# Kernel optimization log

Hardware: AMD Instinct MI355X
Metric: run time of the kernel (lower is better)

## Reference

```python
import jax, jax.numpy as jnp
import numpy as np

NEG_INF = -1e30  # stands in for -inf on the H-diagonal (matches softmax zeroing)


def conv1x1(x, W, b):
    # x: [B,C,H,W], W: [O,C], b: [O] -> [B,O,H,W]
    return jnp.einsum('bchw,oc->bohw', x, W) + b[None, :, None, None]


def setup_inputs() -> dict:
    key = jax.random.key(0)
    ks = jax.random.split(key, 8)
    B, C, H, W = 4, 64, 256, 256
    C8 = C // 8
    s = 1.0 / np.sqrt(C)
    return {
        'x': jax.random.normal(ks[0], (B, C, H, W), jnp.float32),
        'Wq': jax.random.normal(ks[1], (C8, C), jnp.float32) * s,
        'bq': jnp.zeros((C8,), jnp.float32),
        'Wk': jax.random.normal(ks[2], (C8, C), jnp.float32) * s,
        'bk': jnp.zeros((C8,), jnp.float32),
        'Wv': jax.random.normal(ks[3], (C, C), jnp.float32) * s,
        'bv': jnp.zeros((C,), jnp.float32),
        'gamma': jnp.zeros((1,), jnp.float32),
    }


def reference(x, Wq, bq, Wk, bk, Wv, bv, gamma):
    B, C, H, W = x.shape
    q = conv1x1(x, Wq, bq)   # [B,C8,H,W]
    k = conv1x1(x, Wk, bk)   # [B,C8,H,W]
    v = conv1x1(x, Wv, bv)   # [B,C,H,W]

    # Row (height-axis) attention energies with -inf on the self (diagonal) entry.
    energy_H = jnp.einsum('bchw,bcjw->bhwj', q, k)               # [B,H,W,H]
    diag = jnp.eye(H, dtype=bool)[:, None, :]                    # [H,1,H]
    energy_H = jnp.where(diag[None], NEG_INF, energy_H)
    # Column (width-axis) attention energies.
    energy_W = jnp.einsum('bchw,bchj->bhwj', q, k)               # [B,H,W,W]

    att = jax.nn.softmax(jnp.concatenate([energy_H, energy_W], axis=3), axis=3)
    att_H, att_W = att[..., :H], att[..., H:]                    # [B,H,W,H], [B,H,W,W]

    out_H = jnp.einsum('bcjw,bhwj->bchw', v, att_H)
    out_W = jnp.einsum('bchj,bhwj->bchw', v, att_W)
    return gamma[0] * (out_H + out_W) + x
```

## Files before the change

kernel.cpp:

```cpp
#include <hip/hip_runtime.h>

#define Bn 4
#define Cn 64
#define Hn 256
#define Wn 256
#define HWn 65536

typedef unsigned int u32;
typedef __attribute__((ext_vector_type(2))) unsigned int u32x2;
typedef __attribute__((ext_vector_type(8))) short bf16x8;
typedef __attribute__((ext_vector_type(4))) float f32x4;
typedef __attribute__((ext_vector_type(16))) float f32x16;

__device__ __forceinline__ unsigned short f2b(float f) {
    union { float f; unsigned u; } v; v.f = f;
    return (unsigned short)(v.u >> 16);
}
__device__ __forceinline__ float b2f(unsigned short s) {
    union { float f; unsigned u; } v; v.u = ((unsigned)s) << 16;
    return v.f;
}
__device__ __forceinline__ u32 cvtpk(float lo, float hi) {
    u32 r;
    asm("v_cvt_pk_bf16_f32 %0, %1, %2" : "=v"(r) : "v"(lo), "v"(hi));
    return r;
}
__device__ __forceinline__ void vswap(u32& a, u32& b) {
    asm volatile("v_permlane32_swap_b32 %0, %1" : "+v"(a), "+v"(b));
}
__device__ __forceinline__ float pair_other(float v, int lane) {
    union { float f; u32 u; } A; A.f = v;
    u32 a = A.u, b = A.u;
    vswap(a, b);
    union { u32 u; float f; } R; R.u = (lane < 32) ? b : a;
    return R.f;
}
__device__ __forceinline__ bf16x8 expPack(const f32x16& e, int base, float& ss) {
    float p0 = __expf(e[base + 0]), p1 = __expf(e[base + 1]);
    u32 A = cvtpk(p0, p1); ss += p0 + p1;
    float p4 = __expf(e[base + 4]), p5 = __expf(e[base + 5]);
    u32 B = cvtpk(p4, p5); ss += p4 + p5;
    vswap(A, B);
    float p2 = __expf(e[base + 2]), p3 = __expf(e[base + 3]);
    u32 C = cvtpk(p2, p3); ss += p2 + p3;
    float p6 = __expf(e[base + 6]), p7 = __expf(e[base + 7]);
    u32 D = cvtpk(p6, p7); ss += p6 + p7;
    vswap(C, D);
    union { u32 w[4]; bf16x8 v; } u;
    u.w[0] = A; u.w[1] = C; u.w[2] = B; u.w[3] = D;
    return u.v;
}

__global__ __launch_bounds__(256) void k_proj(
    const float* __restrict__ x,
    const float* __restrict__ Wq, const float* __restrict__ bq,
    const float* __restrict__ Wk, const float* __restrict__ bk,
    const float* __restrict__ Wv, const float* __restrict__ bv,
    unsigned short* __restrict__ qbr, unsigned short* __restrict__ kbr,
    unsigned short* __restrict__ v_row)
{
    __shared__ __align__(16) char Xl[2][16384];
    int t = threadIdx.x, lane = t & 63, wv = t >> 6;
    int row16 = lane & 15, g = lane >> 4;
    int u0 = blockIdx.x * 4;

    bf16x8 Af[5][2];
    #pragma unroll
    for (int m = 0; m < 5; ++m) {
        const float* wrow;
        if (m == 0) wrow = (row16 < 8) ? (Wq + row16 * 64) : (Wk + (row16 - 8) * 64);
        else        wrow = Wv + (size_t)((m - 1) * 16 + row16) * 64;
        #pragma unroll
        for (int ks = 0; ks < 2; ++ks) {
            int c0 = ks * 32 + g * 8;
            f32x4 w0 = *(const f32x4*)(wrow + c0);
            f32x4 w1 = *(const f32x4*)(wrow + c0 + 4);
            bf16x8 a;
            a[0] = (short)f2b(w0[0]); a[1] = (short)f2b(w0[1]);
            a[2] = (short)f2b(w0[2]); a[3] = (short)f2b(w0[3]);
            a[4] = (short)f2b(w1[0]); a[5] = (short)f2b(w1[1]);
            a[6] = (short)f2b(w1[2]); a[7] = (short)f2b(w1[3]);
            Af[m][ks] = a;
        }
    }

    int px4 = (t & 31) * 4;
    int cbase = (t >> 5) << 2;

    f32x4 st[2][8];
    {
        int u = u0;
        int b = u >> 9, rest = u & 511, h = rest >> 1, half = rest & 1;
        const float* xb2 = x + (size_t)b * Cn * HWn + (size_t)h * Wn + half * 128;
        #pragma unroll
        for (int pass = 0; pass < 2; ++pass) {
            int c0s = cbase + pass * 32;
            #pragma unroll
            for (int j = 0; j < 4; ++j)
                st[0][pass * 4 + j] = *(const f32x4*)(xb2 + (size_t)(c0s + j) * HWn + px4);
        }
    }

    #pragma unroll
    for (int ui = 0; ui < 4; ++ui) {
        int u = u0 + ui;
        int b = u >> 9, rest = u & 511, h = rest >> 1, half = rest & 1;
        int cur = ui & 1;

        #pragma unroll
        for (int pass = 0; pass < 2; ++pass) {
            int c0s = cbase + pass * 32;
            #pragma unroll
            for (int i = 0; i < 4; ++i) {
                int px = px4 + i;
                u32x2 w;
                w[0] = (u32)f2b(st[cur][pass * 4 + 0][i]) | ((u32)f2b(st[cur][pass * 4 + 1][i]) << 16);
                w[1] = (u32)f2b(st[cur][pass * 4 + 2][i]) | ((u32)f2b(st[cur][pass * 4 + 3][i]) << 16);
                unsigned addr = (unsigned)(px * 128)
                              + (((unsigned)(c0s * 2)) ^ ((((unsigned)px >> 3) & 7) << 4));
                *(u32x2*)(Xl[cur] + addr) = w;
            }
        }
        __syncthreads();

        if (ui < 3) {
            int un = u + 1;
            int bn = un >> 9, restn = un & 511, hn = restn >> 1, halfn = restn & 1;
            const float* xb2 = x + (size_t)bn * Cn * HWn + (size_t)hn * Wn + halfn * 128;
            #pragma unroll
            for (int pass = 0; pass < 2; ++pass) {
                int c0s = cbase + pass * 32;
                #pragma unroll
                for (int j = 0; j < 4; ++j)
                    st[cur ^ 1][pass * 4 + j] = *(const f32x4*)(xb2 + (size_t)(c0s + j) * HWn + px4);
            }
        }

        f32x4 acc[5][2];
        #pragma unroll
        for (int m = 0; m < 5; ++m)
            #pragma unroll
            for (int nt = 0; nt < 2; ++nt)
                acc[m][nt] = (f32x4){0.f, 0.f, 0.f, 0.f};

        #pragma unroll
        for (int nt = 0; nt < 2; ++nt) {
            int px = wv * 32 + nt * 16 + row16;
            #pragma unroll
            for (int ks = 0; ks < 2; ++ks) {
                int c0 = ks * 32 + g * 8;
                unsigned addr = (unsigned)(px * 128)
                              + (((unsigned)(c0 * 2)) ^ ((((unsigned)px >> 3) & 7) << 4));
                bf16x8 bf = *(const bf16x8*)(Xl[cur] + addr);
                #pragma unroll
                for (int m = 0; m < 5; ++m)
                    acc[m][nt] = __builtin_amdgcn_mfma_f32_16x16x32_bf16(Af[m][ks], bf, acc[m][nt], 0, 0, 0);
            }
        }

        f32x4 bQK = (g < 2) ? *(const f32x4*)(bq + g * 4)
                            : *(const f32x4*)(bk + (g - 2) * 4);
        #pragma unroll
        for (int nt = 0; nt < 2; ++nt) {
            int p = half * 128 + wv * 32 + nt * 16 + row16;
            f32x4 d = acc[0][nt];
            d[0] += bQK[0]; d[1] += bQK[1]; d[2] += bQK[2]; d[3] += bQK[3];
            u32 w0 = (u32)f2b(d[0]) | ((u32)f2b(d[1]) << 16);
            u32 w1 = (u32)f2b(d[2]) | ((u32)f2b(d[3]) << 16);
            size_t roff = ((size_t)(b * Hn + h) * Wn + p) * 8 + (size_t)((g & 1) * 4);
            if (g < 2) {
                *(u32*)(qbr + roff) = w0; *(u32*)(qbr + roff + 2) = w1;
            } else {
                *(u32*)(kbr + roff) = w0; *(u32*)(kbr + roff + 2) = w1;
            }
            #pragma unroll
            for (int m = 1; m < 5; ++m) {
                f32x4 bV = *(const f32x4*)(bv + (m - 1) * 16 + g * 4);
                unsigned short* vp = v_row + (size_t)b * Cn * HWn
                                   + (size_t)((m - 1) * 16 + g * 4) * HWn
                                   + (size_t)h * Wn + p;
                #pragma unroll
                for (int r = 0; r < 4; ++r)
                    vp[(size_t)r * HWn] = f2b(acc[m][nt][r] + bV[r]);
            }
        }
    }
}

__global__ __launch_bounds__(256) void k_tr_bf16(
    const unsigned short* __restrict__ in, unsigned short* __restrict__ out,
    int R, int Ccols)
{
    __shared__ unsigned short tile[64][66];
    int t = threadIdx.x;
    int lr = t >> 6, lc = t & 63;
    int tilesC = Ccols >> 6;
    int per_b = (R >> 6) * tilesC;
    int bid = blockIdx.x;
    int b = bid / per_b;
    int rem = bid - b * per_b;
    int r0 = (rem / tilesC) << 6;
    int c0 = (rem - (rem / tilesC) * tilesC) << 6;
    const unsigned short* ip = in + (size_t)b * R * Ccols;
    unsigned short* op = out + (size_t)b * R * Ccols;
    #pragma unroll
    for (int i = 0; i < 16; ++i) {
        int r = lr * 16 + i;
        tile[r][lc] = ip[(size_t)(r0 + r) * Ccols + c0 + lc];
    }
    __syncthreads();
    #pragma unroll
    for (int i = 0; i < 16; ++i) {
        int c = lr * 16 + i;
        op[(size_t)(c0 + c) * R + r0 + lc] = tile[lc][c];
    }
}

__global__ __launch_bounds__(256, 2) void k_attnH(
    const unsigned short* __restrict__ qbr, const unsigned short* __restrict__ kbr,
    const unsigned short* __restrict__ vT,
    unsigned short* __restrict__ ohp,
    float* __restrict__ sH)
{
    __shared__ __align__(16) unsigned short Vl[16384];
    int t = threadIdx.x, lane = t & 63, wv = t >> 6;
    int l31 = lane & 31, hi = lane >> 5;
    int bid = blockIdx.x;
    int qh = bid & 1;
    int rest = bid >> 1, b = rest >> 8, w = rest & 255;

    const char* vsrc = (const char*)(vT + ((size_t)(b * Wn + w)) * Cn * Hn);
    #pragma unroll
    for (int p = 0; p < 8; ++p) {
        int lin = p * 4096 + t * 16;
        int c = lin >> 9;
        f32x4 d = *(const f32x4*)(vsrc + lin);
        unsigned dst = (unsigned)lin ^ ((unsigned)(c & 7) << 4);
        *(f32x4*)((char*)Vl + dst) = d;
    }

    bf16x8 zer = {};
    int qtA = qh * 4 + wv;
    int q = qtA * 32 + l31;
    bf16x8 Qf, Kf[8];
    {
        bf16x8 v = *(const bf16x8*)(qbr + ((size_t)(b * Hn + q) * Wn + w) * 8);
        Qf = (hi == 0) ? v : zer;
    }
    #pragma unroll
    for (int jt = 0; jt < 8; ++jt) {
        int j = jt * 32 + l31;
        bf16x8 v = *(const bf16x8*)(kbr + ((size_t)(b * Hn + j) * Wn + w) * 8);
        Kf[jt] = (hi == 0) ? v : zer;
    }
    __syncthreads();

    f32x16 Oa = {}, Ob = {};
    float s = 0.f;
    #pragma unroll
    for (int jt = 0; jt < 8; ++jt) {
        f32x16 zc = {};
        f32x16 e = __builtin_amdgcn_mfma_f32_32x32x16_bf16(Kf[jt], Qf, zc, 0, 0, 0);
        if (jt == qtA) {
            #pragma unroll
            for (int r = 0; r < 16; ++r) {
                int rl = (r & 3) + 8 * (r >> 2) + 4 * hi;
                e[r] = (rl == l31) ? -1e30f : e[r];
            }
        }
        bf16x8 P0 = expPack(e, 0, s);
        bf16x8 P1 = expPack(e, 8, s);
        #pragma unroll
        for (int k2 = 0; k2 < 2; ++k2) {
            int ktA = jt * 2 + k2;
            bf16x8 Pf = k2 ? P1 : P0;
            #pragma unroll
            for (int ct = 0; ct < 2; ++ct) {
                int c = ct * 32 + l31;
                unsigned ad = ((unsigned)(c * 512 + ktA * 32 + hi * 16))
                            ^ ((unsigned)(c & 7) << 4);
                bf16x8 Vf = *(const bf16x8*)((const char*)Vl + ad);
                if (ct == 0) Oa = __builtin_amdgcn_mfma_f32_32x32x16_bf16(Vf, Pf, Oa, 0, 0, 0);
                else         Ob = __builtin_amdgcn_mfma_f32_32x32x16_bf16(Vf, Pf, Ob, 0, 0, 0);
            }
        }
    }
    float s_tot = s + pair_other(s, lane);
    if (hi == 0) {
        size_t so = ((size_t)(b * Wn + w)) * Hn + q;
        sH[so] = s_tot;
    }
    unsigned short* ob = ohp + (((size_t)(b * Wn + w) * Hn + q) * Cn);
    #pragma unroll
    for (int ct = 0; ct < 2; ++ct) {
        #pragma unroll
        for (int rq = 0; rq < 4; ++rq) {
            int c0 = ct * 32 + rq * 8 + 4 * hi;
            const f32x16& O = ct ? Ob : Oa;
            u32x2 wv2;
            wv2[0] = cvtpk(O[rq * 4 + 0], O[rq * 4 + 1]);
            wv2[1] = cvtpk(O[rq * 4 + 2], O[rq * 4 + 3]);
            *(u32x2*)(ob + c0) = wv2;
        }
    }
}

__global__ __launch_bounds__(256, 2) void k_attnW(
    const unsigned short* __restrict__ qbr, const unsigned short* __restrict__ kbr,
    const unsigned short* __restrict__ v_row,
    const unsigned short* __restrict__ ohp,
    const float* __restrict__ sH,
    const float* __restrict__ x, const float* __restrict__ gamma,
    float* __restrict__ out)
{
    __shared__ __align__(16) unsigned short Vl[16384];
    int t = threadIdx.x, lane = t & 63, wv = t >> 6;
    int l31 = lane & 31, hi = lane >> 5;
    int bid = blockIdx.x;
    int qh = bid & 1;
    int rest = bid >> 1, b = rest >> 8, h = rest & 255;

    #pragma unroll
    for (int p = 0; p < 8; ++p) {
        int lin = p * 4096 + t * 16;
        int c = lin >> 9, off = lin & 511;
        const char* src = (const char*)(v_row + ((size_t)(b * Cn + c)) * HWn + (size_t)h * Wn) + off;
        f32x4 d = *(const f32x4*)src;
        unsigned dst = (unsigned)lin ^ ((unsigned)(c & 7) << 4);
        *(f32x4*)((char*)Vl + dst) = d;
    }

    const unsigned short* qb = qbr + ((size_t)(b * Hn + h)) * Wn * 8;
    const unsigned short* kb = kbr + ((size_t)(b * Hn + h)) * Wn * 8;
    bf16x8 zer = {};
    int q = qh * 128 + wv * 32 + l31;
    bf16x8 Qf, Kf[8];
    {
        bf16x8 v = *(const bf16x8*)(qb + (size_t)q * 8);
        Qf = (hi == 0) ? v : zer;
    }
    #pragma unroll
    for (int jt = 0; jt < 8; ++jt) {
        int j = jt * 32 + l31;
        bf16x8 v = *(const bf16x8*)(kb + (size_t)j * 8);
        Kf[jt] = (hi == 0) ? v : zer;
    }
    float g = gamma[0];
    __syncthreads();

    f32x16 Oa = {}, Ob = {};
    float s = 0.f;
    #pragma unroll
    for (int jt = 0; jt < 8; ++jt) {
        f32x16 zc = {};
        f32x16 e = __builtin_amdgcn_mfma_f32_32x32x16_bf16(Kf[jt], Qf, zc, 0, 0, 0);
        bf16x8 P0 = expPack(e, 0, s);
        bf16x8 P1 = expPack(e, 8, s);
        #pragma unroll
        for (int k2 = 0; k2 < 2; ++k2) {
            int ktA = jt * 2 + k2;
            bf16x8 Pf = k2 ? P1 : P0;
            #pragma unroll
            for (int ct = 0; ct < 2; ++ct) {
                int c = ct * 32 + l31;
                unsigned ad = ((unsigned)(c * 512 + ktA * 32 + hi * 16))
                            ^ ((unsigned)(c & 7) << 4);
                bf16x8 Vf = *(const bf16x8*)((const char*)Vl + ad);
                if (ct == 0) Oa = __builtin_amdgcn_mfma_f32_32x32x16_bf16(Vf, Pf, Oa, 0, 0, 0);
                else         Ob = __builtin_amdgcn_mfma_f32_32x32x16_bf16(Vf, Pf, Ob, 0, 0, 0);
            }
        }
    }
    float s_tot = s + pair_other(s, lane);
    size_t so = ((size_t)(b * Wn + q)) * Hn + h;
    float sh = sH[so];
    float gi = g / (s_tot + sh);
    const unsigned short* op = ohp + (((size_t)(b * Wn + q) * Hn + h) * Cn);
    #pragma unroll
    for (int ct = 0; ct < 2; ++ct) {
        #pragma unroll
        for (int rq = 0; rq < 4; ++rq) {
            int c0 = ct * 32 + rq * 8 + 4 * hi;
            u32x2 wv2 = *(const u32x2*)(op + c0);
            const f32x16& O = ct ? Ob : Oa;
            #pragma unroll
            for (int j = 0; j < 4; ++j) {
                int c = c0 + j;
                size_t idx = ((size_t)(b * Cn + c) * Hn + h) * Wn + q;
                unsigned short oh16 = (unsigned short)((wv2[j >> 1] >> ((j & 1) * 16)) & 0xffff);
                out[idx] = gi * (O[rq * 4 + j] + b2f(oh16)) + x[idx];
            }
        }
    }
}

extern "C" void kernel_launch(void* const* d_in, const int* in_sizes, int n_in,
                              void* d_out, int out_size, void* d_ws, size_t ws_size,
                              hipStream_t stream) {
    const float* x  = (const float*)d_in[0];
    const float* Wq = (const float*)d_in[1];
    const float* bq = (const float*)d_in[2];
    const float* Wk = (const float*)d_in[3];
    const float* bk = (const float*)d_in[4];
    const float* Wv = (const float*)d_in[5];
    const float* bv = (const float*)d_in[6];
    const float* gm = (const float*)d_in[7];
    float* out = (float*)d_out;
    char* ws = (char*)d_ws;

    const size_t BHW = (size_t)Bn * Hn * Wn;
    unsigned short* qbr = (unsigned short*)ws;
    unsigned short* kbr = qbr + 8 * BHW;
    unsigned short* v_row = kbr + 8 * BHW;
    unsigned short* vT    = v_row + 64 * BHW;
    unsigned short* ohp   = vT + 64 * BHW;
    float* sHb = (float*)(ohp + 64 * BHW);

    k_proj<<<512, 256, 0, stream>>>(x, Wq, bq, Wk, bk, Wv, bv,
                                    qbr, kbr, v_row);
    k_tr_bf16<<<Bn * (16384 / 64) * (256 / 64), 256, 0, stream>>>(v_row, vT, 16384, 256);
    k_attnH<<<Bn * Wn * 2, 256, 0, stream>>>(qbr, kbr, vT, ohp, sHb);
    k_attnW<<<Bn * Hn * 2, 256, 0, stream>>>(qbr, kbr, v_row, ohp, sHb, x, gm, out);
}
```

Measured before the change: 108.1 us.

## Merge query halves into 512-thread blocks and stage K in shared memory

Each attention block now covers all 256 queries of a column or row with 8 waves instead of two blocks of 4 waves. This halves the redundant V tile loads into LDS per (b,w)/(b,h). K vectors are loaded once into shared memory and read per jt instead of being held as 8 register fragments, which cuts register pressure. Launch bounds are raised to 512 threads with a higher occupancy target. The trade-offs are an extra LDS read per MFMA step and fewer, larger blocks.

```diff
diff --git a/kernel.cpp b/kernel.cpp
--- a/kernel.cpp
+++ b/kernel.cpp
@@ -216,51 +216,50 @@
     }
 }
 
-__global__ __launch_bounds__(256, 2) void k_attnH(
+__global__ __launch_bounds__(512, 6) void k_attnH(
     const unsigned short* __restrict__ qbr, const unsigned short* __restrict__ kbr,
     const unsigned short* __restrict__ vT,
     unsigned short* __restrict__ ohp,
     float* __restrict__ sH)
 {
     __shared__ __align__(16) unsigned short Vl[16384];
+    __shared__ __align__(16) unsigned short Kl[2048];
     int t = threadIdx.x, lane = t & 63, wv = t >> 6;
     int l31 = lane & 31, hi = lane >> 5;
     int bid = blockIdx.x;
-    int qh = bid & 1;
-    int rest = bid >> 1, b = rest >> 8, w = rest & 255;
+    int b = bid >> 8, w = bid & 255;
 
     const char* vsrc = (const char*)(vT + ((size_t)(b * Wn + w)) * Cn * Hn);
     #pragma unroll
-    for (int p = 0; p < 8; ++p) {
-        int lin = p * 4096 + t * 16;
+    for (int p = 0; p < 4; ++p) {
+        int lin = p * 8192 + t * 16;
         int c = lin >> 9;
         f32x4 d = *(const f32x4*)(vsrc + lin);
         unsigned dst = (unsigned)lin ^ ((unsigned)(c & 7) << 4);
         *(f32x4*)((char*)Vl + dst) = d;
     }
+    if (t < 256) {
+        *(bf16x8*)(Kl + t * 8) = *(const bf16x8*)(kbr + ((size_t)(b * Hn + t) * Wn + w) * 8);
+    }
 
     bf16x8 zer = {};
-    int qtA = qh * 4 + wv;
+    int qtA = wv;
     int q = qtA * 32 + l31;
-    bf16x8 Qf, Kf[8];
+    bf16x8 Qf;
     {
         bf16x8 v = *(const bf16x8*)(qbr + ((size_t)(b * Hn + q) * Wn + w) * 8);
         Qf = (hi == 0) ? v : zer;
     }
-    #pragma unroll
-    for (int jt = 0; jt < 8; ++jt) {
-        int j = jt * 32 + l31;
-        bf16x8 v = *(const bf16x8*)(kbr + ((size_t)(b * Hn + j) * Wn + w) * 8);
-        Kf[jt] = (hi == 0) ? v : zer;
-    }
     __syncthreads();
 
     f32x16 Oa = {}, Ob = {};
     float s = 0.f;
     #pragma unroll
     for (int jt = 0; jt < 8; ++jt) {
+        bf16x8 Kfc = *(const bf16x8*)(Kl + (jt * 32 + l31) * 8);
+        if (hi) Kfc = zer;
         f32x16 zc = {};
-        f32x16 e = __builtin_amdgcn_mfma_f32_32x32x16_bf16(Kf[jt], Qf, zc, 0, 0, 0);
+        f32x16 e = __builtin_amdgcn_mfma_f32_32x32x16_bf16(Kfc, Qf, zc, 0, 0, 0);
         if (jt == qtA) {
             #pragma unroll
             for (int r = 0; r < 16; ++r) {
@@ -305,7 +304,7 @@
     }
 }
 
-__global__ __launch_bounds__(256, 2) void k_attnW(
+__global__ __launch_bounds__(512, 6) void k_attnW(
     const unsigned short* __restrict__ qbr, const unsigned short* __restrict__ kbr,
     const unsigned short* __restrict__ v_row,
     const unsigned short* __restrict__ ohp,
@@ -314,37 +313,34 @@
     float* __restrict__ out)
 {
     __shared__ __align__(16) unsigned short Vl[16384];
+    __shared__ __align__(16) unsigned short Kl[2048];
     int t = threadIdx.x, lane = t & 63, wv = t >> 6;
     int l31 = lane & 31, hi = lane >> 5;
     int bid = blockIdx.x;
-    int qh = bid & 1;
-    int rest = bid >> 1, b = rest >> 8, h = rest & 255;
-
-    #pragma unroll
-    for (int p = 0; p < 8; ++p) {
-        int lin = p * 4096 + t * 16;
+    int b = bid >> 8, h = bid & 255;
+
+    #pragma unroll
+    for (int p = 0; p < 4; ++p) {
+        int lin = p * 8192 + t * 16;
         int c = lin >> 9, off = lin & 511;
         const char* src = (const char*)(v_row + ((size_t)(b * Cn + c)) * HWn + (size_t)h * Wn) + off;
         f32x4 d = *(const f32x4*)src;
         unsigned dst = (unsigned)lin ^ ((unsigned)(c & 7) << 4);
         *(f32x4*)((char*)Vl + dst) = d;
     }
-
     const unsigned short* qb = qbr + ((size_t)(b * Hn + h)) * Wn * 8;
     const unsigned short* kb = kbr + ((size_t)(b * Hn + h)) * Wn * 8;
+    if (t < 256) {
+        *(bf16x8*)(Kl + t * 8) = *(const bf16x8*)(kb + (size_t)t * 8);
+    }
+
     bf16x8 zer = {};
-    int q = qh * 128 + wv * 32 + l31;
-    bf16x8 Qf, Kf[8];
+    int q = wv * 32 + l31;
+    bf16x8 Qf;
     {
         bf16x8 v = *(const bf16x8*)(qb + (size_t)q * 8);
         Qf = (hi == 0) ? v : zer;
     }
-    #pragma unroll
-    for (int jt = 0; jt < 8; ++jt) {
-        int j = jt * 32 + l31;
-        bf16x8 v = *(const bf16x8*)(kb + (size_t)j * 8);
-        Kf[jt] = (hi == 0) ? v : zer;
-    }
     float g = gamma[0];
     __syncthreads();
 
@@ -352,8 +348,10 @@
     float s = 0.f;
     #pragma unroll
     for (int jt = 0; jt < 8; ++jt) {
+        bf16x8 Kfc = *(const bf16x8*)(Kl + (jt * 32 + l31) * 8);
+        if (hi) Kfc = zer;
         f32x16 zc = {};
-        f32x16 e = __builtin_amdgcn_mfma_f32_32x32x16_bf16(Kf[jt], Qf, zc, 0, 0, 0);
+        f32x16 e = __builtin_amdgcn_mfma_f32_32x32x16_bf16(Kfc, Qf, zc, 0, 0, 0);
         bf16x8 P0 = expPack(e, 0, s);
         bf16x8 P1 = expPack(e, 8, s);
         #pragma unroll
@@ -419,6 +417,6 @@
     k_proj<<<512, 256, 0, stream>>>(x, Wq, bq, Wk, bk, Wv, bv,
                                     qbr, kbr, v_row);
     k_tr_bf16<<<Bn * (16384 / 64) * (256 / 64), 256, 0, stream>>>(v_row, vT, 16384, 256);
-    k_attnH<<<Bn * Wn * 2, 256, 0, stream>>>(qbr, kbr, vT, ohp, sHb);
-    k_attnW<<<Bn * Hn * 2, 256, 0, stream>>>(qbr, kbr, v_row, ohp, sHb, x, gm, out);
-}
+    k_attnH<<<Bn * Wn, 512, 0, stream>>>(qbr, kbr, vT, ohp, sHb);
+    k_attnW<<<Bn * Hn, 512, 0, stream>>>(qbr, kbr, v_row, ohp, sHb, x, gm, out);
+}
```

Measured after the change: 288.7 us. 2.67x slower.
